# Optimization experiments

Measured on AMD Instinct MI355X. Metric: run time of the kernel, lower is better.

## Reference

```python
import jax, jax.numpy as jnp
import numpy as np

N = 50000      # nodes
E = 1250000    # edges (avg degree 32)
D = 64         # in_channels == hidden_channels
L = 3          # num_layers
IMPROVED_FILL = 2.0  # GCNConv(improved=True) self-loop weight


def setup_inputs() -> dict:
    key = jax.random.key(0)
    ks = jax.random.split(key, 6)
    x = jax.random.normal(ks[0], (N, D), dtype=jnp.float32)
    edge_index = jax.random.randint(ks[1], (2, E), 0, N, dtype=jnp.int64)
    edge_weight = jax.random.uniform(ks[2], (E,), dtype=jnp.float32)
    Ws = jax.random.normal(ks[3], (L, D, D), dtype=jnp.float32) / np.sqrt(D).astype(np.float32)
    bs = jnp.zeros((L, D), dtype=jnp.float32)
    Wf = jax.random.normal(ks[4], (D, 1), dtype=jnp.float32) / np.sqrt(D).astype(np.float32)
    bf = jnp.zeros((1,), dtype=jnp.float32)
    return dict(x=x, edge_index=edge_index, edge_weight=edge_weight,
                Ws=Ws, bs=bs, Wf=Wf, bf=bf, prob=0)


def _gcn_norm(edge_index, edge_weight, n):
    # add self-loops with fill value 2.0 (improved=True)
    loop = jnp.arange(n, dtype=edge_index.dtype)
    row = jnp.concatenate([edge_index[0], loop])  # source nodes (x_j)
    col = jnp.concatenate([edge_index[1], loop])  # target nodes (aggregation)
    w = jnp.concatenate([edge_weight,
                         jnp.full((n,), IMPROVED_FILL, edge_weight.dtype)])
    deg = jax.ops.segment_sum(w, col, num_segments=n)
    dis = jnp.where(deg > 0, jax.lax.rsqrt(deg), 0.0)  # deg^{-1/2}, inf->0
    norm = dis[row] * w * dis[col]                      # [E+N]
    return row, col, norm


def reference(x, edge_index, edge_weight, Ws, bs, Wf, bf, prob):
    n = x.shape[0]
    # gcn_norm depends only on graph structure; compute once, reuse per layer
    row, col, norm = _gcn_norm(edge_index, edge_weight, n)
    for l in range(Ws.shape[0]):
        h = x @ Ws[l]                                  # [N, D] linear transform
        msg = h[row] * norm[:, None]                   # gather + per-edge scale
        agg = jax.ops.segment_sum(msg, col, num_segments=n)  # scatter-add
        x = jax.nn.relu(agg + bs[l])
    # F.dropout(x, p=prob) with prob=0 -> identity (inference)
    return x @ Wf + bf                                 # [N, 1]
```

## Files before the change

kernel.cpp:

```cpp
#include <hip/hip_runtime.h>
#include <hip/hip_bf16.h>

#define DCH 64
#define NB_CSR 256

typedef __attribute__((ext_vector_type(8))) short bfrag;
typedef __attribute__((ext_vector_type(4))) float ffrag;

static __device__ __forceinline__ unsigned short f2bf(float f) {
    unsigned u = __float_as_uint(f);
    unsigned r = (u + 0x7fffu + ((u >> 16) & 1u)) >> 16;
    return (unsigned short)r;
}
static __device__ __forceinline__ float bf2f(unsigned short s) {
    return __uint_as_float(((unsigned)s) << 16);
}

__global__ __launch_bounds__(1024) void histrank_k(const int* __restrict__ col,
                                                   unsigned char* __restrict__ hist,
                                                   unsigned char* __restrict__ lrank,
                                                   int n, int e) {
    __shared__ unsigned bins[12544];
    int B = blockIdx.x, tid = threadIdx.x;
    int chunk = (e + NB_CSR - 1) / NB_CSR;
    int beg = B * chunk;
    int end = min(e, beg + chunk);
    int len = end - beg;
    int n4 = (n + 3) >> 2;
    for (int i = tid; i < n4; i += 1024) bins[i] = 0;
    __syncthreads();
    for (int i = tid; i < len; i += 1024) {
        int c = col[beg + i];
        unsigned sh = (c & 3) * 8;
        unsigned old = atomicAdd(&bins[c >> 2], 1u << sh);
        lrank[beg + i] = (unsigned char)((old >> sh) & 0xffu);
    }
    __syncthreads();
    unsigned* hrow32 = (unsigned*)(hist + (size_t)B * n);
    for (int i = tid; i < n4; i += 1024) hrow32[i] = bins[i];
}

__global__ __launch_bounds__(256) void hist2_k(unsigned char* __restrict__ hist,
                                               int* __restrict__ cnt, int n) {
    int g = blockIdx.x * 256 + threadIdx.x;
    int ng = n >> 2;
    if (g < ng) {
        unsigned r0 = 0, r1 = 0, r2 = 0, r3 = 0;
        size_t stride = (size_t)n >> 2;
        unsigned* p = (unsigned*)hist + g;
#pragma unroll 1
        for (int B = 0; B < NB_CSR; B += 4) {
            unsigned v0 = p[0], v1 = p[stride], v2 = p[2 * stride], v3 = p[3 * stride];
            p[0]          = (r0 & 255) | ((r1 & 255) << 8) | ((r2 & 255) << 16) | ((r3 & 255) << 24);
            r0 += v0 & 255; r1 += (v0 >> 8) & 255; r2 += (v0 >> 16) & 255; r3 += (v0 >> 24) & 255;
            p[stride]     = (r0 & 255) | ((r1 & 255) << 8) | ((r2 & 255) << 16) | ((r3 & 255) << 24);
            r0 += v1 & 255; r1 += (v1 >> 8) & 255; r2 += (v1 >> 16) & 255; r3 += (v1 >> 24) & 255;
            p[2 * stride] = (r0 & 255) | ((r1 & 255) << 8) | ((r2 & 255) << 16) | ((r3 & 255) << 24);
            r0 += v2 & 255; r1 += (v2 >> 8) & 255; r2 += (v2 >> 16) & 255; r3 += (v2 >> 24) & 255;
            p[3 * stride] = (r0 & 255) | ((r1 & 255) << 8) | ((r2 & 255) << 16) | ((r3 & 255) << 24);
            r0 += v3 & 255; r1 += (v3 >> 8) & 255; r2 += (v3 >> 16) & 255; r3 += (v3 >> 24) & 255;
            p += 4 * stride;
        }
        *(int4*)(cnt + 4 * g) = make_int4((int)r0, (int)r1, (int)r2, (int)r3);
    } else if (g == ng) {
        for (int b = ng << 2; b < n; ++b) {
            unsigned run = 0;
            for (int B = 0; B < NB_CSR; ++B) {
                unsigned char* p = hist + (size_t)B * n + b;
                unsigned v = *p; *p = (unsigned char)run; run += v;
            }
            cnt[b] = (int)run;
        }
    }
}

__global__ __launch_bounds__(1024) void scan1_k(const int* __restrict__ cnt,
                                                int* __restrict__ ptr,
                                                int* __restrict__ bsum, int n) {
    __shared__ int wtot[16];
    int tid = threadIdx.x, lane = tid & 63, w = tid >> 6;
    int i = blockIdx.x * 1024 + tid;
    int v = (i < n) ? cnt[i] : 0;
    int s = v;
#pragma unroll
    for (int off = 1; off < 64; off <<= 1) {
        int t = __shfl_up(s, off);
        if (lane >= off) s += t;
    }
    if (lane == 63) wtot[w] = s;
    __syncthreads();
    if (w == 0) {
        int t16 = (lane < 16) ? wtot[lane] : 0;
        int ss = t16;
#pragma unroll
        for (int off = 1; off < 16; off <<= 1) {
            int t = __shfl_up(ss, off);
            if (lane >= off) ss += t;
        }
        if (lane < 16) wtot[lane] = ss - t16;
    }
    __syncthreads();
    int excl = s - v + wtot[w];
    if (i < n) ptr[i] = excl;
    if (tid == 1023) bsum[blockIdx.x] = excl + v;
}

__global__ __launch_bounds__(64) void scan2_k(int* __restrict__ bsum, int nb) {
    int lane = threadIdx.x;
    int v = (lane < nb) ? bsum[lane] : 0;
    int s = v;
#pragma unroll
    for (int off = 1; off < 64; off <<= 1) {
        int t = __shfl_up(s, off);
        if (lane >= off) s += t;
    }
    if (lane < nb) bsum[lane] = s - v;
    if (lane == 63) bsum[nb] = s;
}

__global__ __launch_bounds__(1024) void scan3_k(int* __restrict__ ptr,
                                                const int* __restrict__ bsum,
                                                int n, int nb) {
    int i = blockIdx.x * 1024 + threadIdx.x;
    if (i < n) ptr[i] += bsum[blockIdx.x];
    if (i == 0) ptr[n] = bsum[nb];
}

__global__ __launch_bounds__(256) void place_k(const int* __restrict__ row,
                                               const int* __restrict__ col,
                                               const float* __restrict__ ew,
                                               const int* __restrict__ ptr,
                                               const unsigned char* __restrict__ hist,
                                               const unsigned char* __restrict__ lrank,
                                               uint2* __restrict__ edg,
                                               int chunk, int n, int e) {
    int i = blockIdx.x * 256 + threadIdx.x;
    if (i >= e) return;
    int B = i / chunk;
    int c = col[i];
    int p = ptr[c] + (int)hist[(size_t)B * n + c] + (int)lrank[i];
    edg[p] = make_uint2((unsigned)row[i], __float_as_uint(ew[i]));
}

__global__ __launch_bounds__(256) void deg_k(const int* __restrict__ ptr,
                                             const uint2* __restrict__ edg,
                                             float* __restrict__ dis, int n) {
    int node = blockIdx.x * 4 + (threadIdx.x >> 6);
    int lane = threadIdx.x & 63;
    if (node >= n) return;
    int beg = ptr[node], end = ptr[node + 1];
    float s = 0.f;
    for (int p = beg + lane; p < end; p += 64) s += __uint_as_float(edg[p].y);
#pragma unroll
    for (int off = 32; off > 0; off >>= 1) s += __shfl_down(s, off);
    if (lane == 0) dis[node] = rsqrtf(s + 2.0f);
}

__global__ __launch_bounds__(256) void normw_k(uint2* __restrict__ edg,
                                               const float* __restrict__ dis, int e) {
    int i = blockIdx.x * 256 + threadIdx.x;
    if (i >= e) return;
    uint2 ev = edg[i];
    ((unsigned*)edg)[2 * i + 1] =
        __float_as_uint(__uint_as_float(ev.y) * dis[ev.x]);
}

__global__ __launch_bounds__(256) void pack_k(const float* __restrict__ Ws,
                                              short* __restrict__ wpk, int L) {
    int ent = blockIdx.x * 256 + threadIdx.x;
    if (ent >= L * 512) return;
    int layer = ent >> 9;
    int r = ent & 511;
    int lane = r & 63;
    int st = r >> 6;
    int s = st >> 2, t = st & 3;
    int quad = lane >> 4;
    int ncol = t * 16 + (lane & 15);
    const float* W = Ws + (size_t)layer * DCH * DCH;
    union { short sh[8]; int4 v; } hi, lo;
#pragma unroll
    for (int j = 0; j < 8; ++j) {
        int k = s * 32 + quad * 8 + j;
        float w = W[k * DCH + ncol];
        unsigned short h = f2bf(w);
        hi.sh[j] = (short)h;
        lo.sh[j] = (short)f2bf(w - bf2f(h));
    }
    *(int4*)(wpk + ((size_t)(layer * 2 + 0) * 512 + r) * 8) = hi.v;
    *(int4*)(wpk + ((size_t)(layer * 2 + 1) * 512 + r) * 8) = lo.v;
}

__global__ __launch_bounds__(256) void gemm_k(const float* __restrict__ x,
                                              const short* __restrict__ wpk_layer,
                                              unsigned short* __restrict__ hb, int n_tiles) {
    __shared__ short Wl[2][512 * 8];
    {
        const int4* src = (const int4*)wpk_layer;
        int4* dst = (int4*)&Wl[0][0];
        for (int i = threadIdx.x; i < 1024; i += 256) dst[i] = src[i];
    }
    __syncthreads();
    int wave = threadIdx.x >> 6, lane = threadIdx.x & 63;
    int tile = blockIdx.x * 4 + wave;
    if (tile >= n_tiles) return;
    int m = lane & 15, quad = lane >> 4;
    int row = tile * 16 + m;

    float av[2][8];
    {
        const float4* p0 = (const float4*)(x + (size_t)row * DCH + quad * 8);
        const float4* p1 = (const float4*)(x + (size_t)row * DCH + 32 + quad * 8);
        float4 a0 = p0[0], a1 = p0[1], b0 = p1[0], b1 = p1[1];
        av[0][0] = a0.x; av[0][1] = a0.y; av[0][2] = a0.z; av[0][3] = a0.w;
        av[0][4] = a1.x; av[0][5] = a1.y; av[0][6] = a1.z; av[0][7] = a1.w;
        av[1][0] = b0.x; av[1][1] = b0.y; av[1][2] = b0.z; av[1][3] = b0.w;
        av[1][4] = b1.x; av[1][5] = b1.y; av[1][6] = b1.z; av[1][7] = b1.w;
    }
    bfrag ah[2], al[2];
#pragma unroll
    for (int s = 0; s < 2; ++s)
#pragma unroll
        for (int j = 0; j < 8; ++j) {
            unsigned short hbv = f2bf(av[s][j]);
            ah[s][j] = (short)hbv;
            al[s][j] = (short)f2bf(av[s][j] - bf2f(hbv));
        }

#pragma unroll
    for (int t = 0; t < 4; ++t) {
        ffrag acc = {0.f, 0.f, 0.f, 0.f};
#pragma unroll
        for (int s = 0; s < 2; ++s) {
            bfrag wh = *(bfrag*)&Wl[0][((s * 4 + t) * 64 + lane) * 8];
            bfrag wl = *(bfrag*)&Wl[1][((s * 4 + t) * 64 + lane) * 8];
            acc = __builtin_amdgcn_mfma_f32_16x16x32_bf16(ah[s], wh, acc, 0, 0, 0);
            acc = __builtin_amdgcn_mfma_f32_16x16x32_bf16(al[s], wh, acc, 0, 0, 0);
            acc = __builtin_amdgcn_mfma_f32_16x16x32_bf16(ah[s], wl, acc, 0, 0, 0);
        }
        int colc = t * 16 + m;
#pragma unroll
        for (int r = 0; r < 4; ++r)
            hb[(size_t)(tile * 16 + quad * 4 + r) * DCH + colc] = f2bf(acc[r]);
    }
}

static __device__ __forceinline__ void gather_node(int node, int lane, int p, int hf,
                                                   float dis_c,
                                                   const int* __restrict__ ptr,
                                                   const uint2* __restrict__ edg,
                                                   const unsigned* __restrict__ hbf,
                                                   float& A0, float& A1) {
    float a0 = 0.f, a1 = 0.f;
    if (hf == 0) {
        unsigned sv = hbf[(size_t)node * 32 + p];
        a0 = 2.0f * dis_c * __uint_as_float(sv << 16);
        a1 = 2.0f * dis_c * __uint_as_float(sv & 0xffff0000u);
    }
    int beg = ptr[node], end = ptr[node + 1];
    for (int base = beg; base < end; base += 64) {
        int idx = base + lane;
        int rv = 0; float nv = 0.f;
        if (idx < end) {
            uint2 ev = edg[idx];
            rv = (int)ev.x;
            nv = __uint_as_float(ev.y);
        }
        int m = min(64, end - base);
        int steps = (((m + 1) >> 1) + 7) & ~7;
        for (int j0 = 0; j0 < steps; j0 += 8) {
            unsigned hv[8]; float nn[8];
#pragma unroll
            for (int q = 0; q < 8; ++q) {
                int eidx = 2 * (j0 + q) + hf;
                int r = __shfl(rv, eidx);
                nn[q] = __shfl(nv, eidx);
                hv[q] = hbf[(size_t)r * 32 + p];
            }
#pragma unroll
            for (int q = 0; q < 8; ++q) {
                a0 += __uint_as_float(hv[q] << 16) * nn[q];
                a1 += __uint_as_float(hv[q] & 0xffff0000u) * nn[q];
            }
        }
    }
    A0 = a0 + __shfl_xor(a0, 32);
    A1 = a1 + __shfl_xor(a1, 32);
}

__global__ __launch_bounds__(256) void gg_k(const int* __restrict__ ptr,
                                            const uint2* __restrict__ edg,
                                            const float* __restrict__ dis,
                                            const unsigned* __restrict__ hbf,
                                            const float* __restrict__ b,
                                            const short* __restrict__ wpk_next,
                                            unsigned short* __restrict__ hb_out, int n) {
    __shared__ float xs[16][68];
    int w = threadIdx.x >> 6, lane = threadIdx.x & 63;
    int p = lane & 31, hf = lane >> 5;
    int tile = blockIdx.x;
    float2 bv = ((const float2*)b)[p];
#pragma unroll 1
    for (int i = 0; i < 4; ++i) {
        int node = tile * 16 + w * 4 + i;
        if (node < n) {
            float dis_c = dis[node];
            float A0, A1;
            gather_node(node, lane, p, hf, dis_c, ptr, edg, hbf, A0, A1);
            if (hf == 0) {
                xs[w * 4 + i][2 * p]     = fmaxf(dis_c * A0 + bv.x, 0.f);
                xs[w * 4 + i][2 * p + 1] = fmaxf(dis_c * A1 + bv.y, 0.f);
            }
        }
    }
    __syncthreads();
    int m = lane & 15, quad = lane >> 4, t = w;
    bfrag ah[2], al[2];
#pragma unroll
    for (int s = 0; s < 2; ++s)
#pragma unroll
        for (int j = 0; j < 8; ++j) {
            float v = xs[m][s * 32 + quad * 8 + j];
            unsigned short hbv = f2bf(v);
            ah[s][j] = (short)hbv;
            al[s][j] = (short)f2bf(v - bf2f(hbv));
        }
    ffrag acc = {0.f, 0.f, 0.f, 0.f};
#pragma unroll
    for (int s = 0; s < 2; ++s) {
        bfrag wh = *(const bfrag*)(wpk_next + ((size_t)((s * 4 + t) * 64 + lane)) * 8);
        bfrag wl = *(const bfrag*)(wpk_next + ((size_t)(512 + (s * 4 + t) * 64 + lane)) * 8);
        acc = __builtin_amdgcn_mfma_f32_16x16x32_bf16(ah[s], wh, acc, 0, 0, 0);
        acc = __builtin_amdgcn_mfma_f32_16x16x32_bf16(al[s], wh, acc, 0, 0, 0);
        acc = __builtin_amdgcn_mfma_f32_16x16x32_bf16(ah[s], wl, acc, 0, 0, 0);
    }
    int colc = t * 16 + m;
#pragma unroll
    for (int r = 0; r < 4; ++r) {
        int orow = tile * 16 + quad * 4 + r;
        if (orow < n) hb_out[(size_t)orow * DCH + colc] = f2bf(acc[r]);
    }
}

__global__ __launch_bounds__(256) void gf_k(const int* __restrict__ ptr,
                                            const uint2* __restrict__ edg,
                                            const float* __restrict__ dis,
                                            const unsigned* __restrict__ hbf,
                                            const float* __restrict__ b,
                                            const float* __restrict__ Wf,
                                            const float* __restrict__ bf,
                                            float* __restrict__ out, int n) {
    int node = blockIdx.x * 4 + (threadIdx.x >> 6);
    int lane = threadIdx.x & 63;
    if (node >= n) return;
    int p = lane & 31, hf = lane >> 5;
    float dis_c = dis[node];
    float A0, A1;
    gather_node(node, lane, p, hf, dis_c, ptr, edg, hbf, A0, A1);
    float2 bv = ((const float2*)b)[p];
    float2 wv = ((const float2*)Wf)[p];
    float x0 = fmaxf(dis_c * A0 + bv.x, 0.f);
    float x1 = fmaxf(dis_c * A1 + bv.y, 0.f);
    float v = x0 * wv.x + x1 * wv.y;
#pragma unroll
    for (int off = 16; off > 0; off >>= 1) v += __shfl_down(v, off);
    if (lane == 0) out[node] = v + bf[0];
}

extern "C" void kernel_launch(void* const* d_in, const int* in_sizes, int n_in,
                              void* d_out, int out_size, void* d_ws, size_t ws_size,
                              hipStream_t stream) {
    const float* x0 = (const float*)d_in[0];
    const int*   ei = (const int*)d_in[1];
    const float* ew = (const float*)d_in[2];
    const float* Ws = (const float*)d_in[3];
    const float* bs = (const float*)d_in[4];
    const float* Wf = (const float*)d_in[5];
    const float* bf = (const float*)d_in[6];

    const int n = in_sizes[0] / DCH;
    const int e = in_sizes[2];
    const int L = in_sizes[3] / (DCH * DCH);

    const int* row = ei;
    const int* col = ei + e;

    size_t off = 0;
    auto alloc = [&](size_t bytes) {
        off = (off + 255) & ~(size_t)255;
        void* r = (char*)d_ws + off;
        off += bytes;
        return r;
    };
    const int nb_scan = (n + 1023) / 1024;
    int*   cnt  = (int*)  alloc((size_t)n * 4);
    int*   ptr  = (int*)  alloc((size_t)(n + 1) * 4);
    int*   bsum = (int*)  alloc((size_t)(nb_scan + 1) * 4);
    float* dis  = (float*)alloc((size_t)n * 4);
    short* wpk  = (short*)alloc((size_t)L * 2 * 512 * 8 * 2);
    uint2* edg  = (uint2*)alloc((size_t)e * 8);
    unsigned char* lrank = (unsigned char*)alloc((size_t)e);
    size_t szA = (size_t)NB_CSR * n;
    size_t szH = (size_t)2 * n * DCH * 2;
    unsigned char* hist = (unsigned char*)alloc(szA > szH ? szA : szH);
    unsigned short* hb_a = (unsigned short*)hist;
    unsigned short* hb_b = hb_a + (size_t)n * DCH;

    dim3 blk(256);
    const int n_tiles = (n + 15) / 16;
    const int chunk = (e + NB_CSR - 1) / NB_CSR;

    histrank_k<<<dim3(NB_CSR), dim3(1024), 0, stream>>>(col, hist, lrank, n, e);
    hist2_k   <<<dim3((n / 4 + 1 + 255) / 256), blk, 0, stream>>>(hist, cnt, n);
    scan1_k   <<<dim3(nb_scan), dim3(1024), 0, stream>>>(cnt, ptr, bsum, n);
    scan2_k   <<<dim3(1), dim3(64), 0, stream>>>(bsum, nb_scan);
    scan3_k   <<<dim3(nb_scan), dim3(1024), 0, stream>>>(ptr, bsum, n, nb_scan);
    place_k   <<<dim3((e + 255) / 256), blk, 0, stream>>>(row, col, ew, ptr, hist, lrank, edg, chunk, n, e);
    deg_k     <<<dim3((n + 3) / 4), blk, 0, stream>>>(ptr, edg, dis, n);
    normw_k   <<<dim3((e + 255) / 256), blk, 0, stream>>>(edg, dis, e);
    pack_k    <<<dim3((L * 512 + 255) / 256), blk, 0, stream>>>(Ws, wpk, L);

    const size_t wstride = (size_t)2 * 512 * 8;
    gemm_k<<<dim3((n_tiles + 3) / 4), blk, 0, stream>>>(x0, wpk, hb_a, n_tiles);
    gg_k  <<<dim3(n_tiles), blk, 0, stream>>>(ptr, edg, dis, (const unsigned*)hb_a,
                                              bs, wpk + wstride, hb_b, n);
    gg_k  <<<dim3(n_tiles), blk, 0, stream>>>(ptr, edg, dis, (const unsigned*)hb_b,
                                              bs + DCH, wpk + 2 * wstride, hb_a, n);
    gf_k  <<<dim3((n + 3) / 4), blk, 0, stream>>>(ptr, edg, dis, (const unsigned*)hb_a,
                                                  bs + 2 * DCH, Wf, bf, (float*)d_out, n);
}
```

Measured before the change: 256.5 us.

## Gather bf16 neighbor rows with 16-byte loads across eight edge groups

Reworks the neighbor gather so each 64-lane wavefront processes eight edges at once. Eight lanes cover one 128-byte bf16 row with uint4 loads, replacing the old scheme of two edges per step with 4-byte loads per lane. Partial sums are then reduced across the eight groups with xor shuffles. The aim is fewer, wider memory transactions and more edges in flight per step. In exchange each lane holds 8 accumulators, and low-degree nodes waste more lanes because edges are padded to multiples of 16.

```diff
diff --git a/kernel.cpp b/kernel.cpp
--- a/kernel.cpp
+++ b/kernel.cpp
@@ -14,6 +14,12 @@
 }
 static __device__ __forceinline__ float bf2f(unsigned short s) {
     return __uint_as_float(((unsigned)s) << 16);
+}
+static __device__ __forceinline__ void unpack8(uint4 v, float f[8]) {
+    f[0] = __uint_as_float(v.x << 16); f[1] = __uint_as_float(v.x & 0xffff0000u);
+    f[2] = __uint_as_float(v.y << 16); f[3] = __uint_as_float(v.y & 0xffff0000u);
+    f[4] = __uint_as_float(v.z << 16); f[5] = __uint_as_float(v.z & 0xffff0000u);
+    f[6] = __uint_as_float(v.w << 16); f[7] = __uint_as_float(v.w & 0xffff0000u);
 }
 
 __global__ __launch_bounds__(1024) void histrank_k(const int* __restrict__ col,
@@ -244,17 +250,20 @@
     }
 }
 
-static __device__ __forceinline__ void gather_node(int node, int lane, int p, int hf,
-                                                   float dis_c,
-                                                   const int* __restrict__ ptr,
-                                                   const uint2* __restrict__ edg,
-                                                   const unsigned* __restrict__ hbf,
-                                                   float& A0, float& A1) {
-    float a0 = 0.f, a1 = 0.f;
-    if (hf == 0) {
-        unsigned sv = hbf[(size_t)node * 32 + p];
-        a0 = 2.0f * dis_c * __uint_as_float(sv << 16);
-        a1 = 2.0f * dis_c * __uint_as_float(sv & 0xffff0000u);
+static __device__ __forceinline__ void gather_node16(int node, int lane, int sub, int grp,
+                                                     float dis_c,
+                                                     const int* __restrict__ ptr,
+                                                     const uint2* __restrict__ edg,
+                                                     const uint4* __restrict__ hb4,
+                                                     float acc[8]) {
+    if (grp == 0) {
+        float f[8];
+        unpack8(hb4[(size_t)node * 8 + sub], f);
+#pragma unroll
+        for (int q = 0; q < 8; ++q) acc[q] = 2.0f * dis_c * f[q];
+    } else {
+#pragma unroll
+        for (int q = 0; q < 8; ++q) acc[q] = 0.f;
     }
     int beg = ptr[node], end = ptr[node + 1];
     for (int base = beg; base < end; base += 64) {
@@ -266,49 +275,61 @@
             nv = __uint_as_float(ev.y);
         }
         int m = min(64, end - base);
-        int steps = (((m + 1) >> 1) + 7) & ~7;
-        for (int j0 = 0; j0 < steps; j0 += 8) {
-            unsigned hv[8]; float nn[8];
-#pragma unroll
-            for (int q = 0; q < 8; ++q) {
-                int eidx = 2 * (j0 + q) + hf;
-                int r = __shfl(rv, eidx);
-                nn[q] = __shfl(nv, eidx);
-                hv[q] = hbf[(size_t)r * 32 + p];
-            }
-#pragma unroll
-            for (int q = 0; q < 8; ++q) {
-                a0 += __uint_as_float(hv[q] << 16) * nn[q];
-                a1 += __uint_as_float(hv[q] & 0xffff0000u) * nn[q];
-            }
-        }
-    }
-    A0 = a0 + __shfl_xor(a0, 32);
-    A1 = a1 + __shfl_xor(a1, 32);
+        int ns2 = (((m + 7) >> 3) + 1) & ~1;
+        for (int s = 0; s < ns2; s += 2) {
+            int e0 = s * 8 + grp, e1 = e0 + 8;
+            int   r0 = __shfl(rv, e0);
+            float n0 = __shfl(nv, e0);
+            int   r1 = __shfl(rv, e1);
+            float n1 = __shfl(nv, e1);
+            uint4 h0 = hb4[(size_t)r0 * 8 + sub];
+            uint4 h1 = hb4[(size_t)r1 * 8 + sub];
+            float f0[8], f1[8];
+            unpack8(h0, f0); unpack8(h1, f1);
+#pragma unroll
+            for (int q = 0; q < 8; ++q) acc[q] += f0[q] * n0 + f1[q] * n1;
+        }
+    }
+#pragma unroll
+    for (int q = 0; q < 8; ++q) {
+        acc[q] += __shfl_xor(acc[q], 8);
+        acc[q] += __shfl_xor(acc[q], 16);
+        acc[q] += __shfl_xor(acc[q], 32);
+    }
 }
 
 __global__ __launch_bounds__(256) void gg_k(const int* __restrict__ ptr,
                                             const uint2* __restrict__ edg,
                                             const float* __restrict__ dis,
-                                            const unsigned* __restrict__ hbf,
+                                            const uint4* __restrict__ hb4,
                                             const float* __restrict__ b,
                                             const short* __restrict__ wpk_next,
                                             unsigned short* __restrict__ hb_out, int n) {
     __shared__ float xs[16][68];
     int w = threadIdx.x >> 6, lane = threadIdx.x & 63;
-    int p = lane & 31, hf = lane >> 5;
+    int sub = lane & 7, grp = lane >> 3;
     int tile = blockIdx.x;
-    float2 bv = ((const float2*)b)[p];
+    float4 b0 = ((const float4*)b)[sub * 2];
+    float4 b1 = ((const float4*)b)[sub * 2 + 1];
 #pragma unroll 1
     for (int i = 0; i < 4; ++i) {
         int node = tile * 16 + w * 4 + i;
         if (node < n) {
             float dis_c = dis[node];
-            float A0, A1;
-            gather_node(node, lane, p, hf, dis_c, ptr, edg, hbf, A0, A1);
-            if (hf == 0) {
-                xs[w * 4 + i][2 * p]     = fmaxf(dis_c * A0 + bv.x, 0.f);
-                xs[w * 4 + i][2 * p + 1] = fmaxf(dis_c * A1 + bv.y, 0.f);
+            float acc[8];
+            gather_node16(node, lane, sub, grp, dis_c, ptr, edg, hb4, acc);
+            if (grp == 0) {
+                float4 r0, r1;
+                r0.x = fmaxf(dis_c * acc[0] + b0.x, 0.f);
+                r0.y = fmaxf(dis_c * acc[1] + b0.y, 0.f);
+                r0.z = fmaxf(dis_c * acc[2] + b0.z, 0.f);
+                r0.w = fmaxf(dis_c * acc[3] + b0.w, 0.f);
+                r1.x = fmaxf(dis_c * acc[4] + b1.x, 0.f);
+                r1.y = fmaxf(dis_c * acc[5] + b1.y, 0.f);
+                r1.z = fmaxf(dis_c * acc[6] + b1.z, 0.f);
+                r1.w = fmaxf(dis_c * acc[7] + b1.w, 0.f);
+                *(float4*)&xs[w * 4 + i][sub * 8]     = r0;
+                *(float4*)&xs[w * 4 + i][sub * 8 + 4] = r1;
             }
         }
     }
@@ -344,7 +365,7 @@
 __global__ __launch_bounds__(256) void gf_k(const int* __restrict__ ptr,
                                             const uint2* __restrict__ edg,
                                             const float* __restrict__ dis,
-                                            const unsigned* __restrict__ hbf,
+                                            const uint4* __restrict__ hb4,
                                             const float* __restrict__ b,
                                             const float* __restrict__ Wf,
                                             const float* __restrict__ bf,
@@ -352,17 +373,28 @@
     int node = blockIdx.x * 4 + (threadIdx.x >> 6);
     int lane = threadIdx.x & 63;
     if (node >= n) return;
-    int p = lane & 31, hf = lane >> 5;
+    int sub = lane & 7, grp = lane >> 3;
     float dis_c = dis[node];
-    float A0, A1;
-    gather_node(node, lane, p, hf, dis_c, ptr, edg, hbf, A0, A1);
-    float2 bv = ((const float2*)b)[p];
-    float2 wv = ((const float2*)Wf)[p];
-    float x0 = fmaxf(dis_c * A0 + bv.x, 0.f);
-    float x1 = fmaxf(dis_c * A1 + bv.y, 0.f);
-    float v = x0 * wv.x + x1 * wv.y;
-#pragma unroll
-    for (int off = 16; off > 0; off >>= 1) v += __shfl_down(v, off);
+    float acc[8];
+    gather_node16(node, lane, sub, grp, dis_c, ptr, edg, hb4, acc);
+    float v = 0.f;
+    if (grp == 0) {
+        float4 b0 = ((const float4*)b)[sub * 2];
+        float4 b1 = ((const float4*)b)[sub * 2 + 1];
+        float4 w0 = ((const float4*)Wf)[sub * 2];
+        float4 w1 = ((const float4*)Wf)[sub * 2 + 1];
+        v  = fmaxf(dis_c * acc[0] + b0.x, 0.f) * w0.x;
+        v += fmaxf(dis_c * acc[1] + b0.y, 0.f) * w0.y;
+        v += fmaxf(dis_c * acc[2] + b0.z, 0.f) * w0.z;
+        v += fmaxf(dis_c * acc[3] + b0.w, 0.f) * w0.w;
+        v += fmaxf(dis_c * acc[4] + b1.x, 0.f) * w1.x;
+        v += fmaxf(dis_c * acc[5] + b1.y, 0.f) * w1.y;
+        v += fmaxf(dis_c * acc[6] + b1.z, 0.f) * w1.z;
+        v += fmaxf(dis_c * acc[7] + b1.w, 0.f) * w1.w;
+    }
+    v += __shfl_down(v, 4);
+    v += __shfl_down(v, 2);
+    v += __shfl_down(v, 1);
     if (lane == 0) out[node] = v + bf[0];
 }
 
@@ -421,10 +453,10 @@
 
     const size_t wstride = (size_t)2 * 512 * 8;
     gemm_k<<<dim3((n_tiles + 3) / 4), blk, 0, stream>>>(x0, wpk, hb_a, n_tiles);
-    gg_k  <<<dim3(n_tiles), blk, 0, stream>>>(ptr, edg, dis, (const unsigned*)hb_a,
+    gg_k  <<<dim3(n_tiles), blk, 0, stream>>>(ptr, edg, dis, (const uint4*)hb_a,
                                               bs, wpk + wstride, hb_b, n);
-    gg_k  <<<dim3(n_tiles), blk, 0, stream>>>(ptr, edg, dis, (const unsigned*)hb_b,
+    gg_k  <<<dim3(n_tiles), blk, 0, stream>>>(ptr, edg, dis, (const uint4*)hb_b,
                                               bs + DCH, wpk + 2 * wstride, hb_a, n);
-    gf_k  <<<dim3((n + 3) / 4), blk, 0, stream>>>(ptr, edg, dis, (const unsigned*)hb_a,
+    gf_k  <<<dim3((n + 3) / 4), blk, 0, stream>>>(ptr, edg, dis, (const uint4*)hb_a,
                                                   bs + 2 * DCH, Wf, bf, (float*)d_out, n);
 }
```

New measurement: 266.0 us. +3.7%, slower.
